# Optimization experiments

Hardware: AMD Instinct MI355X
Metric: run time of the kernel (lower is better)

Reference implementation:

```python
import jax, jax.numpy as jnp
import numpy as np

NUM_LINKS = 1048576


def _euler_rots(theta):
    # theta: [N,3] -> per-link rotation R = Rz @ Ry @ Rx, shape [N,3,3]
    cx, cy, cz = jnp.cos(theta[:, 0]), jnp.cos(theta[:, 1]), jnp.cos(theta[:, 2])
    sx, sy, sz = jnp.sin(theta[:, 0]), jnp.sin(theta[:, 1]), jnp.sin(theta[:, 2])
    z = jnp.zeros_like(cx)
    o = jnp.ones_like(cx)
    rx = jnp.stack([jnp.stack([o, z, z], -1),
                    jnp.stack([z, cx, -sx], -1),
                    jnp.stack([z, sx, cx], -1)], -2)
    ry = jnp.stack([jnp.stack([cy, z, sy], -1),
                    jnp.stack([z, o, z], -1),
                    jnp.stack([-sy, z, cy], -1)], -2)
    rz = jnp.stack([jnp.stack([cz, -sz, z], -1),
                    jnp.stack([sz, cz, z], -1),
                    jnp.stack([z, z, o], -1)], -2)
    return jnp.matmul(rz, jnp.matmul(ry, rx))  # [N,3,3]


def setup_inputs() -> dict:
    key = jax.random.key(0)
    k1, k2 = jax.random.split(key)
    link_lengths = jax.random.uniform(k1, (NUM_LINKS,), dtype=jnp.float32)
    theta = jax.random.normal(k2, (NUM_LINKS, 3), dtype=jnp.float32)
    return {"link_lengths": link_lengths, "theta": theta}


def reference(link_lengths, theta):
    # Original loop computes eff_pos_i = sum_{j=0..i} (R_0 @ R_1 @ ... @ R_j) @ t_j
    # with t_j = l_j * e_z. Vectorize via prefix matrix products + cumsum.
    R = _euler_rots(theta)                                   # [N,3,3]
    P = jax.lax.associative_scan(jnp.matmul, R)              # P_j = R_0@...@R_j
    v = P[:, :, 2] * link_lengths[:, None]                   # P_j @ (l_j * e_z)
    return jnp.cumsum(v, axis=0)                             # [N,3]
```

## Files before the change

kernel.cpp:

```cpp
#include <hip/hip_runtime.h>
#include <math.h>


#define TPB 256
#define EPT 4
#define EPB (TPB * EPT)
#define MAXB 1024
#define NWAVE (TPB / 64)

struct Xf {
    float m[9];
    float p[3];
};

__device__ __forceinline__ void xf_identity(Xf& x) {
    x.m[0] = 1.f; x.m[1] = 0.f; x.m[2] = 0.f;
    x.m[3] = 0.f; x.m[4] = 1.f; x.m[5] = 0.f;
    x.m[6] = 0.f; x.m[7] = 0.f; x.m[8] = 1.f;
    x.p[0] = 0.f; x.p[1] = 0.f; x.p[2] = 0.f;
}

__device__ __forceinline__ Xf xf_comb(const Xf& A, const Xf& B) {
    Xf o;
#pragma unroll
    for (int r = 0; r < 3; ++r) {
        const float a0 = A.m[r * 3 + 0], a1 = A.m[r * 3 + 1], a2 = A.m[r * 3 + 2];
#pragma unroll
        for (int c = 0; c < 3; ++c) {
            o.m[r * 3 + c] = a0 * B.m[0 * 3 + c] + a1 * B.m[1 * 3 + c] + a2 * B.m[2 * 3 + c];
        }
        o.p[r] = A.p[r] + a0 * B.p[0] + a1 * B.p[1] + a2 * B.p[2];
    }
    return o;
}

__device__ __forceinline__ void fast_sincos(float x, float& s, float& c) {
    const float fn = __builtin_rintf(x * 0.636619772367581343f);
    const int n = (int)fn;
    float r = __builtin_fmaf(fn, -1.57079637050628662109375f, x);
    r = __builtin_fmaf(fn, 4.37113900018624283e-8f, r);
    const float r2 = r * r;
    float sp = __builtin_fmaf(r2, -1.9515295891e-4f, 8.3321608736e-3f);
    sp = __builtin_fmaf(r2, sp, -1.6666654611e-1f);
    const float ss = __builtin_fmaf(r * r2, sp, r);
    float cp = __builtin_fmaf(r2, 2.443315711809948e-5f, -1.388731625493765e-3f);
    cp = __builtin_fmaf(r2, cp, 4.166664568298827e-2f);
    const float cc = __builtin_fmaf(r2 * r2, cp,
                                    __builtin_fmaf(r2, -0.5f, 1.0f));
    const int q = n & 3;
    const float s0 = (q & 1) ? cc : ss;
    const float c0 = (q & 1) ? ss : cc;
    const unsigned sgn_s = (unsigned)(q & 2) << 30;
    const unsigned sgn_c = (unsigned)((q + 1) & 2) << 30;
    s = __uint_as_float(__float_as_uint(s0) ^ sgn_s);
    c = __uint_as_float(__float_as_uint(c0) ^ sgn_c);
}

__device__ __forceinline__ void xf_fold(Xf& a, float ax, float ay, float az, float l) {
    float sx, cx, sy, cy, sz, cz;
    fast_sincos(ax, sx, cx);
    fast_sincos(ay, sy, cy);
    fast_sincos(az, sz, cz);
    const float sysx = sy * sx, sycx = sy * cx;
    const float r00 = cz * cy;
    const float r01 = cz * sysx - sz * cx;
    const float r02 = sz * sx + cz * sycx;
    const float r10 = sz * cy;
    const float r11 = cz * cx + sz * sysx;
    const float r12 = sz * sycx - cz * sx;
    const float r20 = -sy;
    const float r21 = cy * sx;
    const float r22 = cy * cx;
    const float t0 = l * r02, t1 = l * r12, t2 = l * r22;
    const float p0 = a.p[0] + a.m[0] * t0 + a.m[1] * t1 + a.m[2] * t2;
    const float p1 = a.p[1] + a.m[3] * t0 + a.m[4] * t1 + a.m[5] * t2;
    const float p2 = a.p[2] + a.m[6] * t0 + a.m[7] * t1 + a.m[8] * t2;
    const float n0 = a.m[0] * r00 + a.m[1] * r10 + a.m[2] * r20;
    const float n1 = a.m[0] * r01 + a.m[1] * r11 + a.m[2] * r21;
    const float n2 = a.m[0] * r02 + a.m[1] * r12 + a.m[2] * r22;
    const float n3 = a.m[3] * r00 + a.m[4] * r10 + a.m[5] * r20;
    const float n4 = a.m[3] * r01 + a.m[4] * r11 + a.m[5] * r21;
    const float n5 = a.m[3] * r02 + a.m[4] * r12 + a.m[5] * r22;
    const float n6 = a.m[6] * r00 + a.m[7] * r10 + a.m[8] * r20;
    const float n7 = a.m[6] * r01 + a.m[7] * r11 + a.m[8] * r21;
    const float n8 = a.m[6] * r02 + a.m[7] * r12 + a.m[8] * r22;
    a.m[0] = n0; a.m[1] = n1; a.m[2] = n2;
    a.m[3] = n3; a.m[4] = n4; a.m[5] = n5;
    a.m[6] = n6; a.m[7] = n7; a.m[8] = n8;
    a.p[0] = p0; a.p[1] = p1; a.p[2] = p2;
}

template <int CTRL, int RMASK>
__device__ __forceinline__ float dpp_f(float src, float oldv) {
    return __int_as_float(__builtin_amdgcn_update_dpp(
        __float_as_int(oldv), __float_as_int(src), CTRL, RMASK, 0xF, false));
}

template <int CTRL, int RMASK>
__device__ __forceinline__ Xf xf_scan_step(const Xf& v) {
    Xf b;
    b.m[0] = dpp_f<CTRL, RMASK>(v.m[0], 1.f);
    b.m[1] = dpp_f<CTRL, RMASK>(v.m[1], 0.f);
    b.m[2] = dpp_f<CTRL, RMASK>(v.m[2], 0.f);
    b.m[3] = dpp_f<CTRL, RMASK>(v.m[3], 0.f);
    b.m[4] = dpp_f<CTRL, RMASK>(v.m[4], 1.f);
    b.m[5] = dpp_f<CTRL, RMASK>(v.m[5], 0.f);
    b.m[6] = dpp_f<CTRL, RMASK>(v.m[6], 0.f);
    b.m[7] = dpp_f<CTRL, RMASK>(v.m[7], 0.f);
    b.m[8] = dpp_f<CTRL, RMASK>(v.m[8], 1.f);
    b.p[0] = dpp_f<CTRL, RMASK>(v.p[0], 0.f);
    b.p[1] = dpp_f<CTRL, RMASK>(v.p[1], 0.f);
    b.p[2] = dpp_f<CTRL, RMASK>(v.p[2], 0.f);
    return xf_comb(b, v);
}

__device__ __forceinline__ Xf wave_scan(Xf v) {
    v = xf_scan_step<0x111, 0xF>(v);
    v = xf_scan_step<0x112, 0xF>(v);
    v = xf_scan_step<0x114, 0xF>(v);
    v = xf_scan_step<0x118, 0xF>(v);
    v = xf_scan_step<0x142, 0xA>(v);
    v = xf_scan_step<0x143, 0xC>(v);
    return v;
}

__device__ __forceinline__ Xf xf_shfl_up1(const Xf& a) {
    Xf o;
#pragma unroll
    for (int k = 0; k < 9; ++k) o.m[k] = __shfl_up(a.m[k], 1, 64);
#pragma unroll
    for (int k = 0; k < 3; ++k) o.p[k] = __shfl_up(a.p[k], 1, 64);
    return o;
}

__device__ __forceinline__ Xf xf_load4(const Xf* p) {
    const float4* g = (const float4*)p;
    const float4 x = g[0], y = g[1], z = g[2];
    Xf b;
    b.m[0] = x.x; b.m[1] = x.y; b.m[2] = x.z;
    b.m[3] = x.w; b.m[4] = y.x; b.m[5] = y.y;
    b.m[6] = y.z; b.m[7] = y.w; b.m[8] = z.x;
    b.p[0] = z.y; b.p[1] = z.z; b.p[2] = z.w;
    return b;
}
__device__ __forceinline__ void xf_store4(Xf* p, const Xf& b) {
    float4* g = (float4*)p;
    g[0] = make_float4(b.m[0], b.m[1], b.m[2], b.m[3]);
    g[1] = make_float4(b.m[4], b.m[5], b.m[6], b.m[7]);
    g[2] = make_float4(b.m[8], b.p[0], b.p[1], b.p[2]);
}

__device__ __forceinline__ void xf_apply(const Xf& T, float q0, float q1, float q2,
                                         float& o0, float& o1, float& o2) {
    o0 = T.p[0] + T.m[0] * q0 + T.m[1] * q1 + T.m[2] * q2;
    o1 = T.p[1] + T.m[3] * q0 + T.m[4] * q1 + T.m[5] * q2;
    o2 = T.p[2] + T.m[6] * q0 + T.m[7] * q1 + T.m[8] * q2;
}

__device__ __forceinline__ void local_fold(const float* __restrict__ ll,
                                           const float* __restrict__ th,
                                           long long j0, int n, Xf& a,
                                           float pe[EPT][3], bool record) {
    xf_identity(a);
    if (j0 + EPT <= n) {
        const float4* th4 = (const float4*)(th + 3 * j0);
        const float4 A = th4[0], B = th4[1], C = th4[2];
        const float4 L = *(const float4*)(ll + j0);
        xf_fold(a, A.x, A.y, A.z, L.x);
        if (record) { pe[0][0] = a.p[0]; pe[0][1] = a.p[1]; pe[0][2] = a.p[2]; }
        xf_fold(a, A.w, B.x, B.y, L.y);
        if (record) { pe[1][0] = a.p[0]; pe[1][1] = a.p[1]; pe[1][2] = a.p[2]; }
        xf_fold(a, B.z, B.w, C.x, L.z);
        if (record) { pe[2][0] = a.p[0]; pe[2][1] = a.p[1]; pe[2][2] = a.p[2]; }
        xf_fold(a, C.y, C.z, C.w, L.w);
        if (record) { pe[3][0] = a.p[0]; pe[3][1] = a.p[1]; pe[3][2] = a.p[2]; }
    } else {
#pragma unroll
        for (int e = 0; e < EPT; ++e) {
            const long long j = j0 + e;
            if (j < n) xf_fold(a, th[3 * j + 0], th[3 * j + 1], th[3 * j + 2], ll[j]);
            if (record) { pe[e][0] = a.p[0]; pe[e][1] = a.p[1]; pe[e][2] = a.p[2]; }
        }
    }
}

__global__ void __launch_bounds__(TPB, 4)
fk_agg(const float* __restrict__ ll, const float* __restrict__ th,
       Xf* __restrict__ agg, int n) {
    __shared__ Xf wagg[NWAVE];
    const int t = threadIdx.x;
    const int lane = t & 63, w = t >> 6;
    const long long j0 = (long long)blockIdx.x * EPB + (long long)t * EPT;

    Xf a;
    float pe[EPT][3];
    local_fold(ll, th, j0, n, a, pe, false);

    const Xf inc = wave_scan(a);
    if (lane == 63) wagg[w] = inc;
    __syncthreads();

    if (t == 0) {
        Xf acc = wagg[0];
#pragma unroll
        for (int k = 1; k < NWAVE; ++k) acc = xf_comb(acc, wagg[k]);
        xf_store4(&agg[blockIdx.x], acc);
    }
}

__global__ void __launch_bounds__(TPB, 4)
fk_apply(const float* __restrict__ ll, const float* __restrict__ th,
         const Xf* __restrict__ agg, float* __restrict__ out, int n) {
    __shared__ Xf wred[NWAVE];
    __shared__ Xf wagg[NWAVE];
    __shared__ Xf shG;
    const int t = threadIdx.x, bid = blockIdx.x;
    const int lane = t & 63, w = t >> 6;
    const long long j0 = (long long)bid * EPB + (long long)t * EPT;

    {
        const int i0 = t * EPT;
        Xf A;
        xf_identity(A);
#pragma unroll
        for (int e = 0; e < EPT; ++e) {
            const int i = i0 + e;
            if (i < bid) A = xf_comb(A, xf_load4(&agg[i]));
        }
        const Xf inc = wave_scan(A);
        if (lane == 63) wred[w] = inc;
    }
    __syncthreads();
    if (t == 0) {
        Xf G = wred[0];
#pragma unroll
        for (int k = 1; k < NWAVE; ++k) G = xf_comb(G, wred[k]);
        shG = G;
    }

    Xf a;
    float pe[EPT][3];
    local_fold(ll, th, j0, n, a, pe, true);

    const Xf inc = wave_scan(a);
    if (lane == 63) wagg[w] = inc;
    __syncthreads();

    Xf exw;
    xf_identity(exw);
    for (int k = 0; k < w; ++k) exw = xf_comb(exw, wagg[k]);

    const Xf ext = xf_shfl_up1(inc);

    Xf T = xf_comb(shG, exw);
    if (lane != 0) T = xf_comb(T, ext);

    if (j0 + EPT <= n) {
        float o[EPT * 3];
#pragma unroll
        for (int e = 0; e < EPT; ++e)
            xf_apply(T, pe[e][0], pe[e][1], pe[e][2],
                     o[e * 3 + 0], o[e * 3 + 1], o[e * 3 + 2]);
        float4* o4 = (float4*)(out + 3 * j0);
        o4[0] = make_float4(o[0], o[1], o[2], o[3]);
        o4[1] = make_float4(o[4], o[5], o[6], o[7]);
        o4[2] = make_float4(o[8], o[9], o[10], o[11]);
    } else {
#pragma unroll
        for (int e = 0; e < EPT; ++e) {
            const long long j = j0 + e;
            if (j < n) {
                float o0, o1, o2;
                xf_apply(T, pe[e][0], pe[e][1], pe[e][2], o0, o1, o2);
                out[3 * j + 0] = o0; out[3 * j + 1] = o1; out[3 * j + 2] = o2;
            }
        }
    }
}

extern "C" void kernel_launch(void* const* d_in, const int* in_sizes, int n_in,
                              void* d_out, int out_size, void* d_ws, size_t ws_size,
                              hipStream_t stream) {
    const float* ll = (const float*)d_in[0];
    const float* th = (const float*)d_in[1];
    float* out = (float*)d_out;
    const int n = in_sizes[0];

    int nb = (n + EPB - 1) / EPB;
    if (nb > MAXB) nb = MAXB;

    Xf* agg = (Xf*)d_ws;

    fk_agg<<<nb, TPB, 0, stream>>>(ll, th, agg, n);
    fk_apply<<<nb, TPB, 0, stream>>>(ll, th, agg, out, n);
}
```

Baseline: 29.66 us.

## Fuse aggregate and apply kernels into one pass with grouped atomic counters

Merges the two-kernel reduce-then-scan into a single kernel. Each block folds its tile once, publishes its aggregate, then bumps a per-group atomic counter. Wave 0 spin-waits with acquire loads until every earlier group has finished before combining prefixes. This removes the second read of the inputs, the second fold pass and one launch, but adds a memset launch. It relies on all blocks being co-resident (at most 1024 blocks), otherwise the spin-wait could deadlock.

```diff
diff --git a/kernel.cpp b/kernel.cpp
--- a/kernel.cpp
+++ b/kernel.cpp
@@ -7,6 +7,9 @@
 #define EPB (TPB * EPT)
 #define MAXB 1024
 #define NWAVE (TPB / 64)
+#define GRP 32
+#define NGRP (MAXB / GRP)
+#define CNT_STRIDE 32
 
 struct Xf {
     float m[9];
@@ -160,64 +163,75 @@
 __device__ __forceinline__ void local_fold(const float* __restrict__ ll,
                                            const float* __restrict__ th,
                                            long long j0, int n, Xf& a,
-                                           float pe[EPT][3], bool record) {
+                                           float pe[EPT][3]) {
     xf_identity(a);
     if (j0 + EPT <= n) {
         const float4* th4 = (const float4*)(th + 3 * j0);
         const float4 A = th4[0], B = th4[1], C = th4[2];
         const float4 L = *(const float4*)(ll + j0);
         xf_fold(a, A.x, A.y, A.z, L.x);
-        if (record) { pe[0][0] = a.p[0]; pe[0][1] = a.p[1]; pe[0][2] = a.p[2]; }
+        pe[0][0] = a.p[0]; pe[0][1] = a.p[1]; pe[0][2] = a.p[2];
         xf_fold(a, A.w, B.x, B.y, L.y);
-        if (record) { pe[1][0] = a.p[0]; pe[1][1] = a.p[1]; pe[1][2] = a.p[2]; }
+        pe[1][0] = a.p[0]; pe[1][1] = a.p[1]; pe[1][2] = a.p[2];
         xf_fold(a, B.z, B.w, C.x, L.z);
-        if (record) { pe[2][0] = a.p[0]; pe[2][1] = a.p[1]; pe[2][2] = a.p[2]; }
+        pe[2][0] = a.p[0]; pe[2][1] = a.p[1]; pe[2][2] = a.p[2];
         xf_fold(a, C.y, C.z, C.w, L.w);
-        if (record) { pe[3][0] = a.p[0]; pe[3][1] = a.p[1]; pe[3][2] = a.p[2]; }
+        pe[3][0] = a.p[0]; pe[3][1] = a.p[1]; pe[3][2] = a.p[2];
     } else {
 #pragma unroll
         for (int e = 0; e < EPT; ++e) {
             const long long j = j0 + e;
             if (j < n) xf_fold(a, th[3 * j + 0], th[3 * j + 1], th[3 * j + 2], ll[j]);
-            if (record) { pe[e][0] = a.p[0]; pe[e][1] = a.p[1]; pe[e][2] = a.p[2]; }
+            pe[e][0] = a.p[0]; pe[e][1] = a.p[1]; pe[e][2] = a.p[2];
         }
     }
 }
 
 __global__ void __launch_bounds__(TPB, 4)
-fk_agg(const float* __restrict__ ll, const float* __restrict__ th,
-       Xf* __restrict__ agg, int n) {
+fk_onepass(const float* __restrict__ ll, const float* __restrict__ th,
+           Xf* __restrict__ agg, unsigned* __restrict__ cnt,
+           float* __restrict__ out, int n, int nb) {
     __shared__ Xf wagg[NWAVE];
-    const int t = threadIdx.x;
-    const int lane = t & 63, w = t >> 6;
-    const long long j0 = (long long)blockIdx.x * EPB + (long long)t * EPT;
-
-    Xf a;
-    float pe[EPT][3];
-    local_fold(ll, th, j0, n, a, pe, false);
-
-    const Xf inc = wave_scan(a);
-    if (lane == 63) wagg[w] = inc;
-    __syncthreads();
-
-    if (t == 0) {
-        Xf acc = wagg[0];
-#pragma unroll
-        for (int k = 1; k < NWAVE; ++k) acc = xf_comb(acc, wagg[k]);
-        xf_store4(&agg[blockIdx.x], acc);
-    }
-}
-
-__global__ void __launch_bounds__(TPB, 4)
-fk_apply(const float* __restrict__ ll, const float* __restrict__ th,
-         const Xf* __restrict__ agg, float* __restrict__ out, int n) {
     __shared__ Xf wred[NWAVE];
-    __shared__ Xf wagg[NWAVE];
     __shared__ Xf shG;
     const int t = threadIdx.x, bid = blockIdx.x;
     const int lane = t & 63, w = t >> 6;
     const long long j0 = (long long)bid * EPB + (long long)t * EPT;
 
+    Xf a;
+    float pe[EPT][3];
+    local_fold(ll, th, j0, n, a, pe);
+
+    const Xf inc = wave_scan(a);
+    if (lane == 63) wagg[w] = inc;
+    __syncthreads();
+
+    if (t == 0) {
+        Xf acc = wagg[0];
+#pragma unroll
+        for (int k = 1; k < NWAVE; ++k) acc = xf_comb(acc, wagg[k]);
+        xf_store4(&agg[bid], acc);
+        __threadfence();
+        __hip_atomic_fetch_add(&cnt[(bid / GRP) * CNT_STRIDE], 1u,
+                               __ATOMIC_RELEASE, __HIP_MEMORY_SCOPE_AGENT);
+    }
+
+    const int myg = bid / GRP;
+    if (w == 0) {
+        for (;;) {
+            unsigned v = 0, tgt = 0;
+            if (lane <= myg) {
+                v = __hip_atomic_load(&cnt[lane * CNT_STRIDE],
+                                      __ATOMIC_ACQUIRE, __HIP_MEMORY_SCOPE_AGENT);
+                const int rem = nb - lane * GRP;
+                tgt = (unsigned)(rem < GRP ? rem : GRP);
+            }
+            if (__all(v >= tgt)) break;
+            __builtin_amdgcn_s_sleep(8);
+        }
+    }
+    __syncthreads();
+
     {
         const int i0 = t * EPT;
         Xf A;
@@ -227,8 +241,8 @@
             const int i = i0 + e;
             if (i < bid) A = xf_comb(A, xf_load4(&agg[i]));
         }
-        const Xf inc = wave_scan(A);
-        if (lane == 63) wred[w] = inc;
+        const Xf ginc = wave_scan(A);
+        if (lane == 63) wred[w] = ginc;
     }
     __syncthreads();
     if (t == 0) {
@@ -237,13 +251,6 @@
         for (int k = 1; k < NWAVE; ++k) G = xf_comb(G, wred[k]);
         shG = G;
     }
-
-    Xf a;
-    float pe[EPT][3];
-    local_fold(ll, th, j0, n, a, pe, true);
-
-    const Xf inc = wave_scan(a);
-    if (lane == 63) wagg[w] = inc;
     __syncthreads();
 
     Xf exw;
@@ -290,7 +297,8 @@
     if (nb > MAXB) nb = MAXB;
 
     Xf* agg = (Xf*)d_ws;
-
-    fk_agg<<<nb, TPB, 0, stream>>>(ll, th, agg, n);
-    fk_apply<<<nb, TPB, 0, stream>>>(ll, th, agg, out, n);
-}
+    unsigned* cnt = (unsigned*)((char*)d_ws + MAXB * sizeof(Xf));
+
+    hipMemsetAsync(cnt, 0, NGRP * CNT_STRIDE * sizeof(unsigned), stream);
+    fk_onepass<<<nb, TPB, 0, stream>>>(ll, th, agg, cnt, out, n, nb);
+}
```

Result: slower. 71.03 us (+139.5%).
